# Kernel optimization log

Measured on AMD Instinct MI355X. Metric: run time of the kernel, lower is better.

Reference implementation:

```python
import jax, jax.numpy as jnp
import numpy as np

B, N, D, H = 4, 1024, 256, 8
DK = D // H
SCALE = DK ** -0.5


def setup_inputs() -> dict:
    key = jax.random.key(0)
    ks = jax.random.split(key, 13)
    x = jax.random.normal(ks[0], (B, N, D), dtype=jnp.float32)
    edge_bias = jax.random.normal(ks[1], (B, H, N, N), dtype=jnp.float32)
    spatial_bias = jax.random.normal(ks[2], (B, H, N, N), dtype=jnp.float32)
    rank_bias = jax.random.normal(ks[3], (B, H, N, N), dtype=jnp.float32)
    key_padding_mask = jax.random.randint(ks[4], (B, N), 0, 2).astype(jnp.bool_)
    s = D ** -0.5  # torch Linear default init scale approximation
    Wq = jax.random.uniform(ks[5], (D, D), jnp.float32, -s, s)
    bq = jax.random.uniform(ks[6], (D,), jnp.float32, -s, s)
    Wk = jax.random.uniform(ks[7], (D, D), jnp.float32, -s, s)
    bk = jax.random.uniform(ks[8], (D,), jnp.float32, -s, s)
    Wv = jax.random.uniform(ks[9], (D, D), jnp.float32, -s, s)
    bv = jax.random.uniform(ks[10], (D,), jnp.float32, -s, s)
    Wo = jax.random.uniform(ks[11], (D, D), jnp.float32, -s, s)
    bo = jax.random.uniform(ks[12], (D,), jnp.float32, -s, s)
    return {"x": x, "edge_bias": edge_bias, "spatial_bias": spatial_bias,
            "rank_bias": rank_bias, "key_padding_mask": key_padding_mask,
            "Wq": Wq, "bq": bq, "Wk": Wk, "bk": bk, "Wv": Wv, "bv": bv,
            "Wo": Wo, "bo": bo}


def reference(x, edge_bias, spatial_bias, rank_bias, key_padding_mask,
              Wq, bq, Wk, bk, Wv, bv, Wo, bo):
    b, n, _ = x.shape
    # torch Linear: y = x @ W.T + b ; reshape to [B, H, N, d_k]
    Q = (x @ Wq.T + bq).reshape(b, n, H, DK).transpose(0, 2, 1, 3)
    K = (x @ Wk.T + bk).reshape(b, n, H, DK).transpose(0, 2, 1, 3)
    V = (x @ Wv.T + bv).reshape(b, n, H, DK).transpose(0, 2, 1, 3)
    scores = jnp.einsum('bhqd,bhkd->bhqk', Q, K) * SCALE
    scores = scores + edge_bias + spatial_bias + rank_bias
    mask = key_padding_mask[:, None, None, :]  # [B,1,1,N]
    scores = jnp.where(mask, -jnp.inf, scores)
    attn = jax.nn.softmax(scores, axis=-1)
    attn = jnp.nan_to_num(attn, nan=0.0)  # fully-masked rows -> 0
    # dropout omitted (eval mode / dropout=0.0)
    out = jnp.einsum('bhqk,bhkd->bhqd', attn, V)
    out = out.transpose(0, 2, 1, 3).reshape(b, n, D)
    return out @ Wo.T + bo
```

## Files before the change

### kernel.cpp

```cpp
#include <hip/hip_runtime.h>
#include <cstddef>

#define SCALE_F 0.17677669529663687f

__global__ __launch_bounds__(256) void qkv_gemm(
    const float* __restrict__ x,
    const float* __restrict__ Wq, const float* __restrict__ bq,
    const float* __restrict__ Wk, const float* __restrict__ bk,
    const float* __restrict__ Wv, const float* __restrict__ bv,
    float* __restrict__ Qbuf, float* __restrict__ Kbuf, float* __restrict__ Vbuf)
{
    __shared__ float As[64][68];
    __shared__ float Bs[64][68];
    const int i0  = blockIdx.x * 64;
    const int bj  = blockIdx.y;
    const int wsel = bj >> 2;
    const int jb  = (bj & 3) * 64;
    const float* __restrict__ W    = (wsel == 0) ? Wq : (wsel == 1) ? Wk : Wv;
    const float* __restrict__ bias = (wsel == 0) ? bq : (wsel == 1) ? bk : bv;
    float* __restrict__ out        = (wsel == 0) ? Qbuf : (wsel == 1) ? Kbuf : Vbuf;

    const int t  = threadIdx.x;
    const int tr = t >> 4, tc = t & 15;

    float acc[4][4] = {};

    for (int d0 = 0; d0 < 256; d0 += 64) {
        #pragma unroll
        for (int ph = 0; ph < 4; ++ph) {
            int id = ph * 256 + t;
            int r  = id >> 4;
            int c4 = (id & 15) << 2;
            *(float4*)&As[r][c4] = *(const float4*)&x[(size_t)(i0 + r) * 256 + d0 + c4];
            *(float4*)&Bs[r][c4] = *(const float4*)&W[(size_t)(jb + r) * 256 + d0 + c4];
        }
        __syncthreads();
        #pragma unroll 4
        for (int dd = 0; dd < 64; dd += 4) {
            float4 av[4], bv4[4];
            #pragma unroll
            for (int ii = 0; ii < 4; ++ii) av[ii]  = *(float4*)&As[tr + 16*ii][dd];
            #pragma unroll
            for (int jj = 0; jj < 4; ++jj) bv4[jj] = *(float4*)&Bs[tc + 16*jj][dd];
            #pragma unroll
            for (int ii = 0; ii < 4; ++ii)
                #pragma unroll
                for (int jj = 0; jj < 4; ++jj)
                    acc[ii][jj] += av[ii].x*bv4[jj].x + av[ii].y*bv4[jj].y
                                 + av[ii].z*bv4[jj].z + av[ii].w*bv4[jj].w;
        }
        __syncthreads();
    }

    #pragma unroll
    for (int ii = 0; ii < 4; ++ii) {
        int i  = i0 + tr + 16*ii;
        int b_ = i >> 10, n = i & 1023;
        #pragma unroll
        for (int jj = 0; jj < 4; ++jj) {
            int j  = jb + tc + 16*jj;
            int hh = j >> 5, dk = j & 31;
            out[(((size_t)(b_*8 + hh)) * 1024 + n) * 32 + dk] = acc[ii][jj] + bias[j];
        }
    }
}

__global__ __launch_bounds__(256) void attn_kernel(
    const float* __restrict__ Qbuf, const float* __restrict__ Kbuf,
    const float* __restrict__ Vbuf,
    const float* __restrict__ ebias, const float* __restrict__ sbias,
    const float* __restrict__ rbias,
    const int* __restrict__ mask, float* __restrict__ attout)
{
    __shared__ float Osh[4][64][33];
    __shared__ float msh[4][64];
    __shared__ float lsh[4][64];

    const int qb = blockIdx.x, h = blockIdx.y, b = blockIdx.z;
    const int t = threadIdx.x;
    const int w = t >> 6, lane = t & 63;
    const int q  = qb * 64 + lane;
    const int bh = b * 8 + h;

    const float* __restrict__ qp = Qbuf + (size_t)(bh * 1024 + q) * 32;
    float Qs[32];
    #pragma unroll
    for (int i = 0; i < 8; ++i) {
        float4 v = *(const float4*)(qp + 4*i);
        Qs[4*i+0] = v.x * SCALE_F; Qs[4*i+1] = v.y * SCALE_F;
        Qs[4*i+2] = v.z * SCALE_F; Qs[4*i+3] = v.w * SCALE_F;
    }

    float O[32];
    #pragma unroll
    for (int d = 0; d < 32; ++d) O[d] = 0.f;
    float m = -1e38f, l = 0.f;

    const size_t rowbase = (size_t)(bh * 1024 + q) * 1024;
    const float* __restrict__ ebp = ebias + rowbase;
    const float* __restrict__ sbp = sbias + rowbase;
    const float* __restrict__ rbp = rbias + rowbase;
    const int*   __restrict__ mp  = mask + b * 1024;
    const float* __restrict__ Kbase = Kbuf + (size_t)bh * 1024 * 32;
    const float* __restrict__ Vbase = Vbuf + (size_t)bh * 1024 * 32;

    for (int kt = 0; kt < 8; ++kt) {
        const int k0 = w * 256 + kt * 32;
        float s[32];
        #pragma unroll
        for (int i = 0; i < 8; ++i) {
            float4 e4 = *(const float4*)(ebp + k0 + 4*i);
            float4 s4 = *(const float4*)(sbp + k0 + 4*i);
            float4 r4 = *(const float4*)(rbp + k0 + 4*i);
            int4   m4 = *(const int4*)(mp + k0 + 4*i);
            s[4*i+0] = m4.x ? -1e38f : (e4.x + s4.x + r4.x);
            s[4*i+1] = m4.y ? -1e38f : (e4.y + s4.y + r4.y);
            s[4*i+2] = m4.z ? -1e38f : (e4.z + s4.z + r4.z);
            s[4*i+3] = m4.w ? -1e38f : (e4.w + s4.w + r4.w);
        }
        #pragma unroll
        for (int kk = 0; kk < 32; ++kk) {
            const float4* kr = (const float4*)(Kbase + (size_t)(k0 + kk) * 32);
            float dot = 0.f;
            #pragma unroll
            for (int i = 0; i < 8; ++i) {
                float4 kv = kr[i];
                dot += Qs[4*i+0]*kv.x + Qs[4*i+1]*kv.y
                     + Qs[4*i+2]*kv.z + Qs[4*i+3]*kv.w;
            }
            s[kk] += dot;
        }
        float tm = s[0];
        #pragma unroll
        for (int kk = 1; kk < 32; ++kk) tm = fmaxf(tm, s[kk]);
        float mnew = fmaxf(m, tm);
        float sc = __expf(m - mnew);
        m = mnew;
        l *= sc;
        #pragma unroll
        for (int d = 0; d < 32; ++d) O[d] *= sc;
        #pragma unroll
        for (int kk = 0; kk < 32; ++kk) {
            float p = __expf(s[kk] - m);
            l += p;
            const float4* vr = (const float4*)(Vbase + (size_t)(k0 + kk) * 32);
            #pragma unroll
            for (int i = 0; i < 8; ++i) {
                float4 vv = vr[i];
                O[4*i+0] += p * vv.x; O[4*i+1] += p * vv.y;
                O[4*i+2] += p * vv.z; O[4*i+3] += p * vv.w;
            }
        }
    }

    #pragma unroll
    for (int d = 0; d < 32; ++d) Osh[w][lane][d] = O[d];
    msh[w][lane] = m;
    lsh[w][lane] = l;
    __syncthreads();

    const int qhat = t >> 2;
    const int cb   = (t & 3) * 8;
    float m0 = msh[0][qhat], m1 = msh[1][qhat], m2 = msh[2][qhat], m3 = msh[3][qhat];
    float M  = fmaxf(fmaxf(m0, m1), fmaxf(m2, m3));
    float e0 = __expf(m0 - M), e1 = __expf(m1 - M);
    float e2 = __expf(m2 - M), e3 = __expf(m3 - M);
    float L  = lsh[0][qhat]*e0 + lsh[1][qhat]*e1 + lsh[2][qhat]*e2 + lsh[3][qhat]*e3;
    float inv = (M <= -1e37f) ? 0.f : 1.f / L;
    float* __restrict__ op = attout + (size_t)(b * 1024 + qb * 64 + qhat) * 256 + h * 32;
    #pragma unroll
    for (int j0 = 0; j0 < 8; j0 += 4) {
        float4 r;
        r.x = (Osh[0][qhat][cb+j0+0]*e0 + Osh[1][qhat][cb+j0+0]*e1
             + Osh[2][qhat][cb+j0+0]*e2 + Osh[3][qhat][cb+j0+0]*e3) * inv;
        r.y = (Osh[0][qhat][cb+j0+1]*e0 + Osh[1][qhat][cb+j0+1]*e1
             + Osh[2][qhat][cb+j0+1]*e2 + Osh[3][qhat][cb+j0+1]*e3) * inv;
        r.z = (Osh[0][qhat][cb+j0+2]*e0 + Osh[1][qhat][cb+j0+2]*e1
             + Osh[2][qhat][cb+j0+2]*e2 + Osh[3][qhat][cb+j0+2]*e3) * inv;
        r.w = (Osh[0][qhat][cb+j0+3]*e0 + Osh[1][qhat][cb+j0+3]*e1
             + Osh[2][qhat][cb+j0+3]*e2 + Osh[3][qhat][cb+j0+3]*e3) * inv;
        *(float4*)(op + cb + j0) = r;
    }
}

__global__ __launch_bounds__(256) void oproj_gemm(
    const float* __restrict__ A, const float* __restrict__ W,
    const float* __restrict__ bias, float* __restrict__ out)
{
    __shared__ float As[64][68];
    __shared__ float Bs[64][68];
    const int i0 = blockIdx.x * 64;
    const int jb = blockIdx.y * 64;
    const int t  = threadIdx.x;
    const int tr = t >> 4, tc = t & 15;
    float acc[4][4] = {};

    for (int d0 = 0; d0 < 256; d0 += 64) {
        #pragma unroll
        for (int ph = 0; ph < 4; ++ph) {
            int id = ph * 256 + t;
            int r  = id >> 4;
            int c4 = (id & 15) << 2;
            *(float4*)&As[r][c4] = *(const float4*)&A[(size_t)(i0 + r) * 256 + d0 + c4];
            *(float4*)&Bs[r][c4] = *(const float4*)&W[(size_t)(jb + r) * 256 + d0 + c4];
        }
        __syncthreads();
        #pragma unroll 4
        for (int dd = 0; dd < 64; dd += 4) {
            float4 av[4], bv4[4];
            #pragma unroll
            for (int ii = 0; ii < 4; ++ii) av[ii]  = *(float4*)&As[tr + 16*ii][dd];
            #pragma unroll
            for (int jj = 0; jj < 4; ++jj) bv4[jj] = *(float4*)&Bs[tc + 16*jj][dd];
            #pragma unroll
            for (int ii = 0; ii < 4; ++ii)
                #pragma unroll
                for (int jj = 0; jj < 4; ++jj)
                    acc[ii][jj] += av[ii].x*bv4[jj].x + av[ii].y*bv4[jj].y
                                 + av[ii].z*bv4[jj].z + av[ii].w*bv4[jj].w;
        }
        __syncthreads();
    }

    #pragma unroll
    for (int ii = 0; ii < 4; ++ii) {
        int i = i0 + tr + 16*ii;
        #pragma unroll
        for (int jj = 0; jj < 4; ++jj) {
            int j = jb + tc + 16*jj;
            out[(size_t)i * 256 + j] = acc[ii][jj] + bias[j];
        }
    }
}

extern "C" void kernel_launch(void* const* d_in, const int* in_sizes, int n_in,
                              void* d_out, int out_size, void* d_ws, size_t ws_size,
                              hipStream_t stream)
{
    const float* x     = (const float*)d_in[0];
    const float* ebias = (const float*)d_in[1];
    const float* sbias = (const float*)d_in[2];
    const float* rbias = (const float*)d_in[3];
    const int*   mask  = (const int*)d_in[4];
    const float* Wq = (const float*)d_in[5];  const float* bq = (const float*)d_in[6];
    const float* Wk = (const float*)d_in[7];  const float* bk = (const float*)d_in[8];
    const float* Wv = (const float*)d_in[9];  const float* bv = (const float*)d_in[10];
    const float* Wo = (const float*)d_in[11]; const float* bo = (const float*)d_in[12];
    float* out = (float*)d_out;

    float* ws = (float*)d_ws;
    float* Qbuf    = ws;
    float* Kbuf    = ws + 1048576;
    float* Vbuf    = ws + 2097152;
    float* attnout = ws + 3145728;

    qkv_gemm<<<dim3(64, 12), 256, 0, stream>>>(x, Wq, bq, Wk, bk, Wv, bv,
                                               Qbuf, Kbuf, Vbuf);
    attn_kernel<<<dim3(16, 8, 4), 256, 0, stream>>>(Qbuf, Kbuf, Vbuf,
                                                    ebias, sbias, rbias,
                                                    mask, attnout);
    oproj_gemm<<<dim3(64, 4), 256, 0, stream>>>(attnout, Wo, bo, out);
}
```

Baseline: 1.032 ms.

## Split attention keys across 16 lanes per query with shuffle merge and XCD-aware grid

Reworks the attention kernel so each query row is handled by 16 lanes, each covering 64 keys, and merges the partial softmax states with wave shuffles instead of shared memory. The grid becomes 2048 blocks of 16 queries, with block ids mapped so that each XCD handles a contiguous group of batch-heads to improve L2 reuse of K/V. Launch bounds request 4 blocks per SM. Bias rows are now read in 256-byte contiguous chunks per lane rather than strided per-lane rows. The shuffle reduction adds 4 rounds of 34 shuffles, and the 4-block launch bound may cause register spills.

```diff
diff --git a/kernel.cpp b/kernel.cpp
--- a/kernel.cpp
+++ b/kernel.cpp
@@ -65,24 +65,28 @@
     }
 }
 
-__global__ __launch_bounds__(256) void attn_kernel(
+__global__ __launch_bounds__(256, 4) void attn_kernel(
     const float* __restrict__ Qbuf, const float* __restrict__ Kbuf,
     const float* __restrict__ Vbuf,
     const float* __restrict__ ebias, const float* __restrict__ sbias,
     const float* __restrict__ rbias,
     const int* __restrict__ mask, float* __restrict__ attout)
 {
-    __shared__ float Osh[4][64][33];
-    __shared__ float msh[4][64];
-    __shared__ float lsh[4][64];
-
-    const int qb = blockIdx.x, h = blockIdx.y, b = blockIdx.z;
-    const int t = threadIdx.x;
-    const int w = t >> 6, lane = t & 63;
-    const int q  = qb * 64 + lane;
-    const int bh = b * 8 + h;
-
-    const float* __restrict__ qp = Qbuf + (size_t)(bh * 1024 + q) * 32;
+    const int id  = blockIdx.x;
+    const int xcd = id & 7;
+    const int jj_ = id >> 3;
+    const int bh  = xcd * 4 + (jj_ >> 6);
+    const int qb  = jj_ & 63;
+    const int b   = bh >> 3, h = bh & 7;
+
+    const int t    = threadIdx.x;
+    const int w    = t >> 6, lane = t & 63;
+    const int qr   = lane >> 4;
+    const int ks   = lane & 15;
+    const int q    = qb * 16 + w * 4 + qr;
+    const int kbase = ks * 64;
+
+    const float* __restrict__ qp = Qbuf + ((size_t)bh * 1024 + q) * 32;
     float Qs[32];
     #pragma unroll
     for (int i = 0; i < 8; ++i) {
@@ -96,19 +100,19 @@
     for (int d = 0; d < 32; ++d) O[d] = 0.f;
     float m = -1e38f, l = 0.f;
 
-    const size_t rowbase = (size_t)(bh * 1024 + q) * 1024;
-    const float* __restrict__ ebp = ebias + rowbase;
-    const float* __restrict__ sbp = sbias + rowbase;
-    const float* __restrict__ rbp = rbias + rowbase;
-    const int*   __restrict__ mp  = mask + b * 1024;
-    const float* __restrict__ Kbase = Kbuf + (size_t)bh * 1024 * 32;
-    const float* __restrict__ Vbase = Vbuf + (size_t)bh * 1024 * 32;
-
-    for (int kt = 0; kt < 8; ++kt) {
-        const int k0 = w * 256 + kt * 32;
-        float s[32];
-        #pragma unroll
-        for (int i = 0; i < 8; ++i) {
+    const size_t rowbase = ((size_t)bh * 1024 + q) * 1024;
+    const float* __restrict__ ebp = ebias + rowbase + kbase;
+    const float* __restrict__ sbp = sbias + rowbase + kbase;
+    const float* __restrict__ rbp = rbias + rowbase + kbase;
+    const int*   __restrict__ mp  = mask + b * 1024 + kbase;
+    const float* __restrict__ Kb  = Kbuf + ((size_t)bh * 1024 + kbase) * 32;
+    const float* __restrict__ Vb  = Vbuf + ((size_t)bh * 1024 + kbase) * 32;
+
+    for (int kt = 0; kt < 4; ++kt) {
+        const int k0 = kt * 16;
+        float s[16];
+        #pragma unroll
+        for (int i = 0; i < 4; ++i) {
             float4 e4 = *(const float4*)(ebp + k0 + 4*i);
             float4 s4 = *(const float4*)(sbp + k0 + 4*i);
             float4 r4 = *(const float4*)(rbp + k0 + 4*i);
@@ -119,20 +123,23 @@
             s[4*i+3] = m4.w ? -1e38f : (e4.w + s4.w + r4.w);
         }
         #pragma unroll
-        for (int kk = 0; kk < 32; ++kk) {
-            const float4* kr = (const float4*)(Kbase + (size_t)(k0 + kk) * 32);
-            float dot = 0.f;
-            #pragma unroll
-            for (int i = 0; i < 8; ++i) {
-                float4 kv = kr[i];
-                dot += Qs[4*i+0]*kv.x + Qs[4*i+1]*kv.y
-                     + Qs[4*i+2]*kv.z + Qs[4*i+3]*kv.w;
-            }
-            s[kk] += dot;
+        for (int kk = 0; kk < 16; ++kk) {
+            const float4* kr = (const float4*)(Kb + (size_t)(k0 + kk) * 32);
+            float4 k0v = kr[0], k1v = kr[1], k2v = kr[2], k3v = kr[3];
+            float4 k4v = kr[4], k5v = kr[5], k6v = kr[6], k7v = kr[7];
+            float d0 = Qs[0]*k0v.x + Qs[1]*k0v.y + Qs[2]*k0v.z + Qs[3]*k0v.w
+                     + Qs[4]*k1v.x + Qs[5]*k1v.y + Qs[6]*k1v.z + Qs[7]*k1v.w;
+            float d1 = Qs[8]*k2v.x + Qs[9]*k2v.y + Qs[10]*k2v.z + Qs[11]*k2v.w
+                     + Qs[12]*k3v.x + Qs[13]*k3v.y + Qs[14]*k3v.z + Qs[15]*k3v.w;
+            float d2 = Qs[16]*k4v.x + Qs[17]*k4v.y + Qs[18]*k4v.z + Qs[19]*k4v.w
+                     + Qs[20]*k5v.x + Qs[21]*k5v.y + Qs[22]*k5v.z + Qs[23]*k5v.w;
+            float d3 = Qs[24]*k6v.x + Qs[25]*k6v.y + Qs[26]*k6v.z + Qs[27]*k6v.w
+                     + Qs[28]*k7v.x + Qs[29]*k7v.y + Qs[30]*k7v.z + Qs[31]*k7v.w;
+            s[kk] += (d0 + d1) + (d2 + d3);
         }
         float tm = s[0];
         #pragma unroll
-        for (int kk = 1; kk < 32; ++kk) tm = fmaxf(tm, s[kk]);
+        for (int kk = 1; kk < 16; ++kk) tm = fmaxf(tm, s[kk]);
         float mnew = fmaxf(m, tm);
         float sc = __expf(m - mnew);
         m = mnew;
@@ -140,10 +147,10 @@
         #pragma unroll
         for (int d = 0; d < 32; ++d) O[d] *= sc;
         #pragma unroll
-        for (int kk = 0; kk < 32; ++kk) {
+        for (int kk = 0; kk < 16; ++kk) {
             float p = __expf(s[kk] - m);
             l += p;
-            const float4* vr = (const float4*)(Vbase + (size_t)(k0 + kk) * 32);
+            const float4* vr = (const float4*)(Vb + (size_t)(k0 + kk) * 32);
             #pragma unroll
             for (int i = 0; i < 8; ++i) {
                 float4 vv = vr[i];
@@ -154,32 +161,31 @@
     }
 
     #pragma unroll
-    for (int d = 0; d < 32; ++d) Osh[w][lane][d] = O[d];
-    msh[w][lane] = m;
-    lsh[w][lane] = l;
-    __syncthreads();
-
-    const int qhat = t >> 2;
-    const int cb   = (t & 3) * 8;
-    float m0 = msh[0][qhat], m1 = msh[1][qhat], m2 = msh[2][qhat], m3 = msh[3][qhat];
-    float M  = fmaxf(fmaxf(m0, m1), fmaxf(m2, m3));
-    float e0 = __expf(m0 - M), e1 = __expf(m1 - M);
-    float e2 = __expf(m2 - M), e3 = __expf(m3 - M);
-    float L  = lsh[0][qhat]*e0 + lsh[1][qhat]*e1 + lsh[2][qhat]*e2 + lsh[3][qhat]*e3;
-    float inv = (M <= -1e37f) ? 0.f : 1.f / L;
-    float* __restrict__ op = attout + (size_t)(b * 1024 + qb * 64 + qhat) * 256 + h * 32;
-    #pragma unroll
-    for (int j0 = 0; j0 < 8; j0 += 4) {
-        float4 r;
-        r.x = (Osh[0][qhat][cb+j0+0]*e0 + Osh[1][qhat][cb+j0+0]*e1
-             + Osh[2][qhat][cb+j0+0]*e2 + Osh[3][qhat][cb+j0+0]*e3) * inv;
-        r.y = (Osh[0][qhat][cb+j0+1]*e0 + Osh[1][qhat][cb+j0+1]*e1
-             + Osh[2][qhat][cb+j0+1]*e2 + Osh[3][qhat][cb+j0+1]*e3) * inv;
-        r.z = (Osh[0][qhat][cb+j0+2]*e0 + Osh[1][qhat][cb+j0+2]*e1
-             + Osh[2][qhat][cb+j0+2]*e2 + Osh[3][qhat][cb+j0+2]*e3) * inv;
-        r.w = (Osh[0][qhat][cb+j0+3]*e0 + Osh[1][qhat][cb+j0+3]*e1
-             + Osh[2][qhat][cb+j0+3]*e2 + Osh[3][qhat][cb+j0+3]*e3) * inv;
-        *(float4*)(op + cb + j0) = r;
+    for (int mk = 1; mk <= 8; mk <<= 1) {
+        float om = __shfl_xor(m, mk, 64);
+        float ol = __shfl_xor(l, mk, 64);
+        float M  = fmaxf(m, om);
+        float a  = __expf(m - M);
+        float bb = __expf(om - M);
+        l = a * l + bb * ol;
+        #pragma unroll
+        for (int d = 0; d < 32; ++d) {
+            float oo = __shfl_xor(O[d], mk, 64);
+            O[d] = a * O[d] + bb * oo;
+        }
+        m = M;
+    }
+
+    if (ks == 0) {
+        float inv = (m <= -1e37f) ? 0.f : 1.f / l;
+        float* __restrict__ op = attout + ((size_t)(b * 1024 + q)) * 256 + h * 32;
+        #pragma unroll
+        for (int i = 0; i < 8; ++i) {
+            float4 r;
+            r.x = O[4*i+0] * inv; r.y = O[4*i+1] * inv;
+            r.z = O[4*i+2] * inv; r.w = O[4*i+3] * inv;
+            *(float4*)(op + 4*i) = r;
+        }
     }
 }
 
@@ -256,8 +262,8 @@
 
     qkv_gemm<<<dim3(64, 12), 256, 0, stream>>>(x, Wq, bq, Wk, bk, Wv, bv,
                                                Qbuf, Kbuf, Vbuf);
-    attn_kernel<<<dim3(16, 8, 4), 256, 0, stream>>>(Qbuf, Kbuf, Vbuf,
-                                                    ebias, sbias, rbias,
-                                                    mask, attnout);
+    attn_kernel<<<2048, 256, 0, stream>>>(Qbuf, Kbuf, Vbuf,
+                                          ebias, sbias, rbias,
+                                          mask, attnout);
     oproj_gemm<<<dim3(64, 4), 256, 0, stream>>>(attnout, Wo, bo, out);
 }
```

Result: slower. 1.401 ms (+35.8%).
